# Performance work log

Hardware: AMD Instinct MI355X
Metric: run time of the kernel (lower is better)

Reference implementation:

```python
import jax, jax.numpy as jnp
import numpy as np

B, T, N, H, DH = 32, 64, 100, 4, 32  # batch, seq, nodes, heads, dim/head


def setup_inputs() -> dict:
    key = jax.random.key(0)
    ks = jax.random.split(key, 20)
    # structured flat observation: [action_mask(132), adj(100*100), dt(1), obs(256), siem(128)]
    am = (jax.random.uniform(ks[0], (B, T, 132)) < 0.8).astype(jnp.float32)
    adj = (jax.random.uniform(ks[1], (B, T, N * N)) < 0.05).astype(jnp.float32)
    dt = jax.random.uniform(ks[2], (B, T, 1)) * 0.1 + 0.01
    obs = jax.random.normal(ks[3], (B, T, 256))
    siem = jax.random.normal(ks[4], (B, T, 128))
    inputs = jnp.concatenate([am, adj, dt, obs, siem], axis=-1)
    s = 0.05
    return dict(
        inputs=inputs,
        h0=jnp.zeros((B, 128), jnp.float32),
        fc_w=jax.random.normal(ks[5], (384, 256)) * s,
        fc_b=jnp.zeros((256,)),
        gat_w=jax.random.normal(ks[6], (256, H, DH)) * s,
        a_src=jax.random.normal(ks[7], (H, DH)) * s,
        a_dst=jax.random.normal(ks[8], (H, DH)) * s,
        ode_w1=jax.random.normal(ks[9], (128, 128)) * s,
        ode_b1=jnp.zeros((128,)),
        ode_w2=jax.random.normal(ks[10], (128, 128)) * s,
        ode_b2=jnp.zeros((128,)),
        gru_wi=jax.random.normal(ks[11], (128, 384)) * s,
        gru_wh=jax.random.normal(ks[12], (128, 384)) * s,
        gru_bi=jnp.zeros((384,)),
        gru_bh=jnp.zeros((384,)),
        act_w=jax.random.normal(ks[13], (128, 132)) * s,
        act_b=jnp.zeros((132,)),
        val_w=jax.random.normal(ks[14], (128, 1)) * s,
        val_b=jnp.zeros((1,)),
    )


def reference(inputs, h0, fc_w, fc_b, gat_w, a_src, a_dst, ode_w1, ode_b1,
              ode_w2, ode_b2, gru_wi, gru_wh, gru_bi, gru_bh, act_w, act_b,
              val_w, val_b):
    Bt, Tt = inputs.shape[0], inputs.shape[1]
    action_mask = inputs[..., :132]
    adj_raw = inputs[..., 132:10132].reshape(Bt * Tt, N, N)
    dtn = inputs[..., 10132:10133]                      # [B,T,1]
    x = jnp.concatenate([inputs[..., 10133:10389], inputs[..., 10389:10517]], -1)
    x = jax.nn.relu(x @ fc_w + fc_b).reshape(Bt * Tt, 256)
    # SubnetMaskGenerator.create_mask: binary adjacency + self loops
    adj = (adj_raw > 0) | jnp.eye(N, dtype=bool)[None]
    # place per-agent embedding at node 0, rest zero
    x_nodes = jnp.zeros((Bt * Tt, N, 256), x.dtype).at[:, 0, :].set(x)
    Wh = jnp.einsum('bnf,fhd->bhnd', x_nodes, gat_w)
    src = jnp.einsum('bhnd,hd->bhn', Wh, a_src)
    dst = jnp.einsum('bhnd,hd->bhn', Wh, a_dst)
    e = jax.nn.leaky_relu(src[:, :, :, None] + dst[:, :, None, :], 0.2)
    e = jnp.where(adj[:, None, :, :], e, -1e9)
    alpha = jax.nn.softmax(e, axis=-1)
    hgat = jax.nn.elu(jnp.einsum('bhij,bhjd->bhid', alpha, Wh))
    hgat = hgat.transpose(0, 2, 1, 3).reshape(Bt * Tt, N, H * DH)
    x_gat = hgat.mean(axis=1).reshape(Bt, Tt, 128)

    def f(h):  # ODE dynamics net
        return jnp.tanh(jnp.tanh(h @ ode_w1 + ode_b1) @ ode_w2 + ode_b2)

    def step(h, inp):
        xt, dt = inp                                    # [B,128], [B,1]
        k1 = f(h)
        k2 = f(h + 0.5 * dt * k1)
        k3 = f(h + 0.5 * dt * k2)
        k4 = f(h + dt * k3)
        h_ode = h + dt / 6.0 * (k1 + 2 * k2 + 2 * k3 + k4)
        gi = xt @ gru_wi + gru_bi
        gh = h_ode @ gru_wh + gru_bh
        ir, iz, inn = jnp.split(gi, 3, -1)
        hr, hz, hn = jnp.split(gh, 3, -1)
        r = jax.nn.sigmoid(ir + hr)
        z = jax.nn.sigmoid(iz + hz)
        n = jnp.tanh(inn + r * hn)
        h_new = (1.0 - z) * n + z * h_ode
        return h_new, h_new

    h_T, hs = jax.lax.scan(step, h0, (x_gat.transpose(1, 0, 2), dtn.transpose(1, 0, 2)))
    x_rnn = hs.transpose(1, 0, 2)                       # [B,T,128]
    logits = x_rnn @ act_w + act_b
    value = (x_rnn @ val_w + val_b).reshape(-1)
    masked_logits = jnp.where(action_mask == 0.0, jnp.float32(-1e10), logits)
    return masked_logits, h_T, value
```

## Files before the change

### kernel.cpp

```cpp
#include <hip/hip_runtime.h>

#define NIN 10517
typedef unsigned short ushort_t;
using f32x4  = __attribute__((ext_vector_type(4))) float;
using bf16x8 = __attribute__((ext_vector_type(8))) short;

__device__ __forceinline__ float lrelu02(float x){ return x > 0.f ? x : 0.2f*x; }
__device__ __forceinline__ float fast_tanh(float x){ float e=__expf(2.f*x); return 1.f - 2.f/(e+1.f); }
__device__ __forceinline__ float fast_sig(float x){ return 1.f/(1.f+__expf(-x)); }

__device__ __forceinline__ ushort_t f2bf(float x){
  unsigned u = __float_as_uint(x);
  unsigned r = u + 0x7FFF + ((u >> 16) & 1);
  return (ushort_t)(r >> 16);
}
__device__ __forceinline__ float bf2f(ushort_t v){ return __uint_as_float(((unsigned)v) << 16); }

#define LBAR() do { asm volatile("s_waitcnt lgkmcnt(0)" ::: "memory"); \
                    __builtin_amdgcn_s_barrier(); } while (0)

__global__ __launch_bounds__(256) void k_fc_gat(const float* __restrict__ inputs,
    const float* __restrict__ fc_w, const float* __restrict__ fc_b,
    const float* __restrict__ gat_w, const float* __restrict__ a_src, const float* __restrict__ a_dst,
    const float* __restrict__ ode_w1, const float* __restrict__ ode_w2, const float* __restrict__ gru_wh,
    const float* __restrict__ act_w, const float* __restrict__ gru_wi,
    float* __restrict__ wh0_ws, float* __restrict__ sd_ws,
    ushort_t* __restrict__ w1B, ushort_t* __restrict__ w2B, ushort_t* __restrict__ ghB,
    ushort_t* __restrict__ actB, ushort_t* __restrict__ wiBt)
{
  __shared__ float xin[8][384];
  __shared__ float xfc[8][256];
  __shared__ float wh[8][128];
  const int tid = threadIdx.x;
  const int bt0 = blockIdx.x * 8;

  for (int p = blockIdx.x * 256 + tid; p < 149504; p += 256*256) {
    if (p < 49152) {
      int m = p >> 7, k = p & 127;
      ghB[p] = f2bf(gru_wh[k*384 + m]);
    } else if (p < 65536) {
      int q = p - 49152, jj = q >> 7, k = q & 127;
      w1B[q] = f2bf(ode_w1[k*128 + jj]);
    } else if (p < 81920) {
      int q = p - 65536, jj = q >> 7, k = q & 127;
      w2B[q] = f2bf(ode_w2[k*128 + jj]);
    } else if (p < 100352) {
      int q = p - 81920, col = q >> 7, k = q & 127;
      actB[q] = (col < 132) ? f2bf(act_w[k*132 + col]) : (ushort_t)0;
    } else {
      int q = p - 100352, m = q >> 7, f = q & 127;
      wiBt[q] = f2bf(gru_wi[f*384 + m]);
    }
  }

  for (int idx = tid; idx < 8*384; idx += 256) {
    int r = idx / 384, f = idx - r*384;
    xin[r][f] = inputs[(size_t)(bt0+r)*NIN + 10133 + f];
  }
  __syncthreads();
  {
    float acc[8];
    float bj = fc_b[tid];
    #pragma unroll
    for (int r=0;r<8;r++) acc[r] = bj;
    for (int f=0; f<384; f++) {
      float wf = fc_w[f*256 + tid];
      #pragma unroll
      for (int r=0;r<8;r++) acc[r] = fmaf(xin[r][f], wf, acc[r]);
    }
    #pragma unroll
    for (int r=0;r<8;r++) xfc[r][tid] = fmaxf(acc[r], 0.f);
  }
  __syncthreads();
  {
    const int j2 = tid & 127, r0 = (tid >> 7) * 4;
    float acc[4];
    #pragma unroll
    for (int r=0;r<4;r++) acc[r] = 0.f;
    for (int f=0; f<256; f++) {
      float wf = gat_w[f*128 + j2];
      #pragma unroll
      for (int r=0;r<4;r++) acc[r] = fmaf(xfc[r0+r][f], wf, acc[r]);
    }
    #pragma unroll
    for (int r=0;r<4;r++) {
      wh[r0+r][j2] = acc[r];
      wh0_ws[(size_t)(bt0+r0+r)*128 + j2] = acc[r];
    }
  }
  __syncthreads();
  if (tid < 64) {
    const int r = tid >> 3, h = (tid >> 1) & 3, w = tid & 1;
    const float* av = w ? a_dst : a_src;
    float acc = 0.f;
    #pragma unroll
    for (int d=0; d<32; d++) acc = fmaf(wh[r][h*32+d], av[h*32+d], acc);
    sd_ws[(size_t)(bt0+r)*8 + w*4 + h] = acc;
  }
}

__global__ __launch_bounds__(256) void k_alpha_gi(const float* __restrict__ inputs,
    const float* __restrict__ wh0_ws, const float* __restrict__ sd_ws,
    ushort_t* __restrict__ xg_bf)
{
  __shared__ int cnt[100];
  __shared__ int a0f[100];
  __shared__ float alpha[4][100];
  __shared__ float wh0[128];
  __shared__ float sdl[8];
  __shared__ float psum[256];
  const int tid = threadIdx.x;
  const size_t bt = blockIdx.x;
  if (tid < 128) wh0[tid] = wh0_ws[bt*128 + tid];
  if (tid < 8) sdl[tid] = sd_ws[bt*8 + tid];
  const float* adj = inputs + bt*NIN + 132;
  const int wv = tid >> 6, lane = tid & 63;
  for (int i = wv; i < 100; i += 4) {
    float v0 = adj[i*100 + lane];
    int pred0 = (lane != 0) && ((v0 > 0.f) || (lane == i));
    unsigned long long b0 = __ballot(pred0);
    int pred1 = 0;
    if (lane < 36) {
      float v1 = adj[i*100 + 64 + lane];
      pred1 = (v1 > 0.f) || ((64 + lane) == i);
    }
    unsigned long long b1 = __ballot(pred1);
    if (lane == 0) {
      cnt[i] = __popcll(b0) + __popcll(b1);
      a0f[i] = (v0 > 0.f) ? 1 : 0;
    }
  }
  __syncthreads();
  for (int idx = tid; idx < 400; idx += 256) {
    int h = idx / 100, i = idx - h*100;
    float s = sdl[h], d = sdl[4+h];
    float a;
    if (i == 0) {
      float ea = __expf(lrelu02(s + d));
      float eb = __expf(lrelu02(s));
      a = ea / (ea + (float)cnt[0] * eb);
    } else if (a0f[i]) {
      float ed = __expf(lrelu02(d));
      a = ed / (ed + (float)cnt[i]);
    } else {
      a = 0.f;
    }
    alpha[h][i] = a;
  }
  __syncthreads();
  {
    const int pr = tid & 127, hf = tid >> 7;
    const float w = wh0[pr];
    const int hh = pr >> 5;
    float sum = 0.f;
    const int i0 = hf * 50;
    for (int i = i0; i < i0 + 50; i++) {
      float t = alpha[hh][i] * w;
      sum += (t > 0.f) ? t : (__expf(t) - 1.f);
    }
    psum[tid] = sum;
  }
  __syncthreads();
  if (tid < 128) xg_bf[bt*128 + tid] = f2bf((psum[tid] + psum[tid+128]) * 0.01f);
}

__global__ __launch_bounds__(512) void k_rnn(const float* __restrict__ inputs,
    const float* __restrict__ h0,
    const ushort_t* __restrict__ w1B, const float* __restrict__ ode_b1,
    const ushort_t* __restrict__ w2B, const float* __restrict__ ode_b2,
    const ushort_t* __restrict__ ghB, const float* __restrict__ gru_bh,
    const ushort_t* __restrict__ actB, const float* __restrict__ act_b,
    const float* __restrict__ val_w, const float* __restrict__ val_b,
    const ushort_t* __restrict__ xg_bf, const ushort_t* __restrict__ wiBt,
    const float* __restrict__ gru_bi,
    float* __restrict__ out_logits, float* __restrict__ out_hT, float* __restrict__ out_val)
{
  __shared__ float gi_lds[64*384];
  __shared__ __align__(16) ushort_t bufA[128];
  __shared__ __align__(16) ushort_t bufB[128];
  __shared__ __align__(16) ushort_t bufC[128];
  __shared__ float dtbuf[64];
  __shared__ __align__(16) ushort_t hsbuf[64*136];
  const int tid = threadIdx.x;
  const int b = blockIdx.x;
  const int w = tid >> 6, lane = tid & 63;
  const int li = lane & 15, g = lane >> 4;
  const int col = w*16 + li;

  {
    const int rt = w & 3, ch = w >> 2;
    bf16x8 haf[4];
    #pragma unroll
    for (int kt=0;kt<4;kt++)
      haf[kt] = *reinterpret_cast<const bf16x8*>(xg_bf + ((size_t)(b*64 + rt*16 + li))*128 + kt*32 + g*8);
    for (int ct = ch*12; ct < ch*12 + 12; ct++) {
      const int m = ct*16 + li;
      const f32x4 z0 = {0.f,0.f,0.f,0.f};
      const ushort_t* wb = wiBt + (size_t)m*128;
      bf16x8 b0 = *reinterpret_cast<const bf16x8*>(wb + 0*32 + g*8);
      bf16x8 b1f = *reinterpret_cast<const bf16x8*>(wb + 1*32 + g*8);
      bf16x8 b2f = *reinterpret_cast<const bf16x8*>(wb + 2*32 + g*8);
      bf16x8 b3f = *reinterpret_cast<const bf16x8*>(wb + 3*32 + g*8);
      f32x4 c0 = __builtin_amdgcn_mfma_f32_16x16x32_bf16(haf[0], b0,  z0, 0,0,0);
      f32x4 c1 = __builtin_amdgcn_mfma_f32_16x16x32_bf16(haf[1], b1f, z0, 0,0,0);
      f32x4 c2 = __builtin_amdgcn_mfma_f32_16x16x32_bf16(haf[2], b2f, z0, 0,0,0);
      f32x4 c3 = __builtin_amdgcn_mfma_f32_16x16x32_bf16(haf[3], b3f, z0, 0,0,0);
      const float bim = gru_bi[m];
      #pragma unroll
      for (int r=0;r<4;r++)
        gi_lds[(rt*16 + g*4 + r)*384 + m] = ((c0[r]+c1[r]) + (c2[r]+c3[r])) + bim;
    }
  }

  const float b1 = ode_b1[col], b2 = ode_b2[col];
  const float bh0 = gru_bh[col], bh1 = gru_bh[col+128], bh2 = gru_bh[col+256];
  float h = h0[b*128 + col];
  if (tid < 64) dtbuf[tid] = inputs[((size_t)b*64 + tid)*NIN + 10132];
  if (lane < 16) bufC[col] = f2bf(h);
  __syncthreads();

  bf16x8 af[4];
  auto ldaf = [&](const ushort_t* __restrict__ hb){
    #pragma unroll
    for (int kt=0;kt<4;kt++) af[kt] = *reinterpret_cast<const bf16x8*>(hb + kt*32 + g*8);
  };
  bf16x8 W1f[4], W2f[4], GAf[4], GBf[4], GCf[4];
  #pragma unroll
  for (int kt=0;kt<4;kt++){
    const int o = kt*32 + g*8;
    W1f[kt] = *reinterpret_cast<const bf16x8*>(w1B + col*128 + o);
    W2f[kt] = *reinterpret_cast<const bf16x8*>(w2B + col*128 + o);
    GAf[kt] = *reinterpret_cast<const bf16x8*>(ghB + (size_t)col*128       + o);
    GBf[kt] = *reinterpret_cast<const bf16x8*>(ghB + (size_t)(col+128)*128 + o);
    GCf[kt] = *reinterpret_cast<const bf16x8*>(ghB + (size_t)(col+256)*128 + o);
  }
  auto mvac = [&](const bf16x8 (&Wf)[4])->float{
    const f32x4 z0 = {0.f,0.f,0.f,0.f};
    f32x4 c0 = __builtin_amdgcn_mfma_f32_16x16x32_bf16(af[0], Wf[0], z0, 0,0,0);
    f32x4 c1 = __builtin_amdgcn_mfma_f32_16x16x32_bf16(af[1], Wf[1], z0, 0,0,0);
    f32x4 c2 = __builtin_amdgcn_mfma_f32_16x16x32_bf16(af[2], Wf[2], z0, 0,0,0);
    f32x4 c3 = __builtin_amdgcn_mfma_f32_16x16x32_bf16(af[3], Wf[3], z0, 0,0,0);
    return (c0[0]+c1[0]) + (c2[0]+c3[0]);
  };

  for (int t=0; t<64; t++) {
    const float dt = dtbuf[t];
    const float gir = gi_lds[t*384 + col];
    const float giz = gi_lds[t*384 + col + 128];
    const float gin = gi_lds[t*384 + col + 256];

    float u, k1, k2, k3, k4;
    ldaf(bufC); u  = fast_tanh(mvac(W1f)+b1); if (lane<16) bufA[col]=f2bf(u);                    LBAR();
    ldaf(bufA); k1 = fast_tanh(mvac(W2f)+b2); if (lane<16) bufB[col]=f2bf(fmaf(0.5f*dt,k1,h));   LBAR();
    ldaf(bufB); u  = fast_tanh(mvac(W1f)+b1); if (lane<16) bufA[col]=f2bf(u);                    LBAR();
    ldaf(bufA); k2 = fast_tanh(mvac(W2f)+b2); if (lane<16) bufB[col]=f2bf(fmaf(0.5f*dt,k2,h));   LBAR();
    ldaf(bufB); u  = fast_tanh(mvac(W1f)+b1); if (lane<16) bufA[col]=f2bf(u);                    LBAR();
    ldaf(bufA); k3 = fast_tanh(mvac(W2f)+b2); if (lane<16) bufB[col]=f2bf(fmaf(dt,k3,h));        LBAR();
    ldaf(bufB); u  = fast_tanh(mvac(W1f)+b1); if (lane<16) bufA[col]=f2bf(u);                    LBAR();
    ldaf(bufA); k4 = fast_tanh(mvac(W2f)+b2);
    const float h_ode = fmaf(dt*(1.f/6.f), (k1 + 2.f*k2) + (2.f*k3 + k4), h);
    if (lane<16) bufB[col] = f2bf(h_ode);                                                        LBAR();

    ldaf(bufB);
    {
      const float r = fast_sig(gir + mvac(GAf) + bh0);
      const float z = fast_sig(giz + mvac(GBf) + bh1);
      const float n = fast_tanh(gin + r*(mvac(GCf) + bh2));
      h = (1.f - z)*n + z*h_ode;
    }
    if (lane < 16) {
      bufC[col] = f2bf(h);
      hsbuf[t*136 + col] = f2bf(h);
    }
    LBAR();
  }

  if (lane < 16) out_hT[b*128 + col] = h;

  {
    const int rt = w & 3, ch = w >> 2;
    const int r0 = rt*16;
    bf16x8 haf[4];
    #pragma unroll
    for (int kt=0;kt<4;kt++)
      haf[kt] = *reinterpret_cast<const bf16x8*>(hsbuf + (r0+li)*136 + kt*32 + g*8);
    const int ct0 = ch ? 5 : 0, ctN = ch ? 9 : 5;
    for (int ct=ct0; ct<ctN; ct++){
      const f32x4 z0 = {0.f,0.f,0.f,0.f};
      f32x4 c0, c1, c2, c3;
      {
        const ushort_t* ab = actB + (size_t)(ct*16+li)*128;
        bf16x8 b0 = *reinterpret_cast<const bf16x8*>(ab + 0*32 + g*8);
        bf16x8 b1f = *reinterpret_cast<const bf16x8*>(ab + 1*32 + g*8);
        bf16x8 b2f = *reinterpret_cast<const bf16x8*>(ab + 2*32 + g*8);
        bf16x8 b3f = *reinterpret_cast<const bf16x8*>(ab + 3*32 + g*8);
        c0 = __builtin_amdgcn_mfma_f32_16x16x32_bf16(haf[0], b0,  z0, 0,0,0);
        c1 = __builtin_amdgcn_mfma_f32_16x16x32_bf16(haf[1], b1f, z0, 0,0,0);
        c2 = __builtin_amdgcn_mfma_f32_16x16x32_bf16(haf[2], b2f, z0, 0,0,0);
        c3 = __builtin_amdgcn_mfma_f32_16x16x32_bf16(haf[3], b3f, z0, 0,0,0);
      }
      const int colL = ct*16 + li;
      if (colL < 132){
        const float ab = act_b[colL];
        #pragma unroll
        for (int reg=0; reg<4; reg++){
          const int r = r0 + g*4 + reg;
          const size_t bt = (size_t)b*64 + r;
          const float mval = inputs[bt*NIN + colL];
          const float v = ((c0[reg]+c1[reg]) + (c2[reg]+c3[reg])) + ab;
          out_logits[bt*132 + colL] = (mval == 0.f) ? -1e10f : v;
        }
      }
    }
  }
  if (tid < 64){
    float acc = val_b[0];
    for (int k=0;k<128;k++) acc = fmaf(bf2f(hsbuf[tid*136 + k]), val_w[k], acc);
    out_val[b*64 + tid] = acc;
  }
}

extern "C" void kernel_launch(void* const* d_in, const int* in_sizes, int n_in,
                              void* d_out, int out_size, void* d_ws, size_t ws_size,
                              hipStream_t stream) {
  (void)in_sizes; (void)n_in; (void)out_size; (void)ws_size;
  const float* inputs = (const float*)d_in[0];
  const float* h0     = (const float*)d_in[1];
  const float* fc_w   = (const float*)d_in[2];
  const float* fc_b   = (const float*)d_in[3];
  const float* gat_w  = (const float*)d_in[4];
  const float* a_src  = (const float*)d_in[5];
  const float* a_dst  = (const float*)d_in[6];
  const float* ode_w1 = (const float*)d_in[7];
  const float* ode_b1 = (const float*)d_in[8];
  const float* ode_w2 = (const float*)d_in[9];
  const float* ode_b2 = (const float*)d_in[10];
  const float* gru_wi = (const float*)d_in[11];
  const float* gru_wh = (const float*)d_in[12];
  const float* gru_bi = (const float*)d_in[13];
  const float* gru_bh = (const float*)d_in[14];
  const float* act_w  = (const float*)d_in[15];
  const float* act_b  = (const float*)d_in[16];
  const float* val_w  = (const float*)d_in[17];
  const float* val_b  = (const float*)d_in[18];

  float* ws   = (float*)d_ws;
  float* wh0  = ws;
  float* sd   = ws + 262144;
  ushort_t* xg_bf = (ushort_t*)(ws + 278528);
  ushort_t* w1B   = (ushort_t*)(ws + 409600);
  ushort_t* w2B   = (ushort_t*)(ws + 417792);
  ushort_t* ghB   = (ushort_t*)(ws + 425984);
  ushort_t* actB  = (ushort_t*)(ws + 450560);
  ushort_t* wiBt  = (ushort_t*)(ws + 459776);

  float* out        = (float*)d_out;
  float* out_logits = out;
  float* out_hT     = out + 270336;
  float* out_val    = out + 274432;

  k_fc_gat  <<<dim3(256),  dim3(256), 0, stream>>>(inputs, fc_w, fc_b, gat_w, a_src, a_dst,
                                                   ode_w1, ode_w2, gru_wh, act_w, gru_wi,
                                                   wh0, sd, w1B, w2B, ghB, actB, wiBt);
  k_alpha_gi<<<dim3(2048), dim3(256), 0, stream>>>(inputs, wh0, sd, xg_bf);
  k_rnn     <<<dim3(32),   dim3(512), 0, stream>>>(inputs, h0, w1B, ode_b1, w2B, ode_b2,
                                                   ghB, gru_bh, actB, act_b, val_w, val_b,
                                                   xg_bf, wiBt, gru_bi,
                                                   out_logits, out_hT, out_val);
}
```

Before: 227.8 us.

## Move GRU input projection into separate parallel kernel writing to workspace

The GRU input-gate projection (x_gat @ gru_wi + bias) was computed inside the 32-block recurrent kernel and stored in a 96KB LDS buffer. It now runs in a new 128-block kernel that writes the result to global workspace, and the recurrent kernel reads it per timestep from global memory. This spreads the projection over more CUs, shortens the serial kernel's prologue and frees its large LDS allocation. In exchange it adds a kernel launch, a global round trip, and global-memory loads inside the timestep loop that may add latency on the critical path.

```diff
diff --git a/kernel.cpp b/kernel.cpp
--- a/kernel.cpp
+++ b/kernel.cpp
@@ -164,6 +164,37 @@
   if (tid < 128) xg_bf[bt*128 + tid] = f2bf((psum[tid] + psum[tid+128]) * 0.01f);
 }
 
+__global__ __launch_bounds__(256) void k_gi(const ushort_t* __restrict__ xg_bf,
+    const ushort_t* __restrict__ wiBt, const float* __restrict__ gru_bi,
+    float* __restrict__ gi_ws)
+{
+  const int tid = threadIdx.x;
+  const int w = tid >> 6, lane = tid & 63;
+  const int li = lane & 15, g = lane >> 4;
+  const int bt0 = blockIdx.x * 16;
+  bf16x8 haf[4];
+  #pragma unroll
+  for (int kt=0;kt<4;kt++)
+    haf[kt] = *reinterpret_cast<const bf16x8*>(xg_bf + ((size_t)(bt0 + li))*128 + kt*32 + g*8);
+  for (int ct = w*6; ct < w*6 + 6; ct++) {
+    const int m = ct*16 + li;
+    const f32x4 z0 = {0.f,0.f,0.f,0.f};
+    const ushort_t* wb = wiBt + (size_t)m*128;
+    bf16x8 b0 = *reinterpret_cast<const bf16x8*>(wb + 0*32 + g*8);
+    bf16x8 b1f = *reinterpret_cast<const bf16x8*>(wb + 1*32 + g*8);
+    bf16x8 b2f = *reinterpret_cast<const bf16x8*>(wb + 2*32 + g*8);
+    bf16x8 b3f = *reinterpret_cast<const bf16x8*>(wb + 3*32 + g*8);
+    f32x4 c0 = __builtin_amdgcn_mfma_f32_16x16x32_bf16(haf[0], b0,  z0, 0,0,0);
+    f32x4 c1 = __builtin_amdgcn_mfma_f32_16x16x32_bf16(haf[1], b1f, z0, 0,0,0);
+    f32x4 c2 = __builtin_amdgcn_mfma_f32_16x16x32_bf16(haf[2], b2f, z0, 0,0,0);
+    f32x4 c3 = __builtin_amdgcn_mfma_f32_16x16x32_bf16(haf[3], b3f, z0, 0,0,0);
+    const float bim = gru_bi[m];
+    #pragma unroll
+    for (int r=0;r<4;r++)
+      gi_ws[(size_t)(bt0 + g*4 + r)*384 + m] = ((c0[r]+c1[r]) + (c2[r]+c3[r])) + bim;
+  }
+}
+
 __global__ __launch_bounds__(512) void k_rnn(const float* __restrict__ inputs,
     const float* __restrict__ h0,
     const ushort_t* __restrict__ w1B, const float* __restrict__ ode_b1,
@@ -171,11 +202,9 @@
     const ushort_t* __restrict__ ghB, const float* __restrict__ gru_bh,
     const ushort_t* __restrict__ actB, const float* __restrict__ act_b,
     const float* __restrict__ val_w, const float* __restrict__ val_b,
-    const ushort_t* __restrict__ xg_bf, const ushort_t* __restrict__ wiBt,
-    const float* __restrict__ gru_bi,
+    const float* __restrict__ gi_ws,
     float* __restrict__ out_logits, float* __restrict__ out_hT, float* __restrict__ out_val)
 {
-  __shared__ float gi_lds[64*384];
   __shared__ __align__(16) ushort_t bufA[128];
   __shared__ __align__(16) ushort_t bufB[128];
   __shared__ __align__(16) ushort_t bufC[128];
@@ -187,43 +216,6 @@
   const int li = lane & 15, g = lane >> 4;
   const int col = w*16 + li;
 
-  {
-    const int rt = w & 3, ch = w >> 2;
-    bf16x8 haf[4];
-    #pragma unroll
-    for (int kt=0;kt<4;kt++)
-      haf[kt] = *reinterpret_cast<const bf16x8*>(xg_bf + ((size_t)(b*64 + rt*16 + li))*128 + kt*32 + g*8);
-    for (int ct = ch*12; ct < ch*12 + 12; ct++) {
-      const int m = ct*16 + li;
-      const f32x4 z0 = {0.f,0.f,0.f,0.f};
-      const ushort_t* wb = wiBt + (size_t)m*128;
-      bf16x8 b0 = *reinterpret_cast<const bf16x8*>(wb + 0*32 + g*8);
-      bf16x8 b1f = *reinterpret_cast<const bf16x8*>(wb + 1*32 + g*8);
-      bf16x8 b2f = *reinterpret_cast<const bf16x8*>(wb + 2*32 + g*8);
-      bf16x8 b3f = *reinterpret_cast<const bf16x8*>(wb + 3*32 + g*8);
-      f32x4 c0 = __builtin_amdgcn_mfma_f32_16x16x32_bf16(haf[0], b0,  z0, 0,0,0);
-      f32x4 c1 = __builtin_amdgcn_mfma_f32_16x16x32_bf16(haf[1], b1f, z0, 0,0,0);
-      f32x4 c2 = __builtin_amdgcn_mfma_f32_16x16x32_bf16(haf[2], b2f, z0, 0,0,0);
-      f32x4 c3 = __builtin_amdgcn_mfma_f32_16x16x32_bf16(haf[3], b3f, z0, 0,0,0);
-      const float bim = gru_bi[m];
-      #pragma unroll
-      for (int r=0;r<4;r++)
-        gi_lds[(rt*16 + g*4 + r)*384 + m] = ((c0[r]+c1[r]) + (c2[r]+c3[r])) + bim;
-    }
-  }
-
-  const float b1 = ode_b1[col], b2 = ode_b2[col];
-  const float bh0 = gru_bh[col], bh1 = gru_bh[col+128], bh2 = gru_bh[col+256];
-  float h = h0[b*128 + col];
-  if (tid < 64) dtbuf[tid] = inputs[((size_t)b*64 + tid)*NIN + 10132];
-  if (lane < 16) bufC[col] = f2bf(h);
-  __syncthreads();
-
-  bf16x8 af[4];
-  auto ldaf = [&](const ushort_t* __restrict__ hb){
-    #pragma unroll
-    for (int kt=0;kt<4;kt++) af[kt] = *reinterpret_cast<const bf16x8*>(hb + kt*32 + g*8);
-  };
   bf16x8 W1f[4], W2f[4], GAf[4], GBf[4], GCf[4];
   #pragma unroll
   for (int kt=0;kt<4;kt++){
@@ -234,6 +226,19 @@
     GBf[kt] = *reinterpret_cast<const bf16x8*>(ghB + (size_t)(col+128)*128 + o);
     GCf[kt] = *reinterpret_cast<const bf16x8*>(ghB + (size_t)(col+256)*128 + o);
   }
+  const float b1 = ode_b1[col], b2 = ode_b2[col];
+  const float bh0 = gru_bh[col], bh1 = gru_bh[col+128], bh2 = gru_bh[col+256];
+  float h = h0[b*128 + col];
+  if (tid < 64) dtbuf[tid] = inputs[((size_t)b*64 + tid)*NIN + 10132];
+  if (lane < 16) bufC[col] = f2bf(h);
+  const float* gib = gi_ws + (size_t)b*64*384 + col;
+  __syncthreads();
+
+  bf16x8 af[4];
+  auto ldaf = [&](const ushort_t* __restrict__ hb){
+    #pragma unroll
+    for (int kt=0;kt<4;kt++) af[kt] = *reinterpret_cast<const bf16x8*>(hb + kt*32 + g*8);
+  };
   auto mvac = [&](const bf16x8 (&Wf)[4])->float{
     const f32x4 z0 = {0.f,0.f,0.f,0.f};
     f32x4 c0 = __builtin_amdgcn_mfma_f32_16x16x32_bf16(af[0], Wf[0], z0, 0,0,0);
@@ -245,9 +250,9 @@
 
   for (int t=0; t<64; t++) {
     const float dt = dtbuf[t];
-    const float gir = gi_lds[t*384 + col];
-    const float giz = gi_lds[t*384 + col + 128];
-    const float gin = gi_lds[t*384 + col + 256];
+    const float gir = gib[(size_t)t*384];
+    const float giz = gib[(size_t)t*384 + 128];
+    const float gin = gib[(size_t)t*384 + 256];
 
     float u, k1, k2, k3, k4;
     ldaf(bufC); u  = fast_tanh(mvac(W1f)+b1); if (lane<16) bufA[col]=f2bf(u);                    LBAR();
@@ -348,11 +353,12 @@
   float* wh0  = ws;
   float* sd   = ws + 262144;
   ushort_t* xg_bf = (ushort_t*)(ws + 278528);
-  ushort_t* w1B   = (ushort_t*)(ws + 409600);
-  ushort_t* w2B   = (ushort_t*)(ws + 417792);
-  ushort_t* ghB   = (ushort_t*)(ws + 425984);
-  ushort_t* actB  = (ushort_t*)(ws + 450560);
-  ushort_t* wiBt  = (ushort_t*)(ws + 459776);
+  float* gi   = ws + 409600;
+  ushort_t* w1B   = (ushort_t*)(ws + 1196032);
+  ushort_t* w2B   = (ushort_t*)(ws + 1204224);
+  ushort_t* ghB   = (ushort_t*)(ws + 1212416);
+  ushort_t* actB  = (ushort_t*)(ws + 1236992);
+  ushort_t* wiBt  = (ushort_t*)(ws + 1246208);
 
   float* out        = (float*)d_out;
   float* out_logits = out;
@@ -363,8 +369,8 @@
                                                    ode_w1, ode_w2, gru_wh, act_w, gru_wi,
                                                    wh0, sd, w1B, w2B, ghB, actB, wiBt);
   k_alpha_gi<<<dim3(2048), dim3(256), 0, stream>>>(inputs, wh0, sd, xg_bf);
+  k_gi      <<<dim3(128),  dim3(256), 0, stream>>>(xg_bf, wiBt, gru_bi, gi);
   k_rnn     <<<dim3(32),   dim3(512), 0, stream>>>(inputs, h0, w1B, ode_b1, w2B, ode_b2,
                                                    ghB, gru_bh, actB, act_b, val_w, val_b,
-                                                   xg_bf, wiBt, gru_bi,
-                                                   out_logits, out_hT, out_val);
-}
+                                                   gi, out_logits, out_hT, out_val);
+}
```

Result: faster. 218.5 us (-4.1%).
